# Optimization experiments

Measured on AMD Instinct MI355X. Metric: run time of the kernel, lower is better.

Reference implementation:

```python
import jax, jax.numpy as jnp
import numpy as np

B, Q, K, H, DQ, DK, DV = 16, 128, 512, 128, 128, 128, 128
MASK_VALUE = -1000000.0  # matches d2l.sequence_mask fill value


def setup_inputs() -> dict:
    key = jax.random.key(0)
    ks = jax.random.split(key, 7)
    queries = jax.random.normal(ks[0], (B, Q, DQ), dtype=jnp.float32)
    keys = jax.random.normal(ks[1], (B, K, DK), dtype=jnp.float32)
    values = jax.random.normal(ks[2], (B, K, DV), dtype=jnp.float32)
    valid_lens = jax.random.randint(ks[3], (B,), 1, K + 1, dtype=jnp.int32)
    # Linear params (no bias), scaled like torch default init ~ 1/sqrt(fan_in)
    W_q = jax.random.normal(ks[4], (DQ, H), dtype=jnp.float32) / np.sqrt(DQ)
    W_k = jax.random.normal(ks[5], (DK, H), dtype=jnp.float32) / np.sqrt(DK)
    w_v = jax.random.normal(ks[6], (H,), dtype=jnp.float32) / np.sqrt(H)
    return {"queries": queries, "keys": keys, "values": values,
            "valid_lens": valid_lens, "W_q": W_q, "W_k": W_k, "w_v": w_v}


def reference(queries, keys, values, valid_lens, W_q, W_k, w_v):
    # Project queries and keys: (B,Q,H), (B,K,H)
    q = jnp.einsum("bqd,dh->bqh", queries, W_q)
    k = jnp.einsum("bkd,dh->bkh", keys, W_k)
    # Broadcast add -> tanh -> linear-to-1 score: (B,Q,K)
    features = jnp.tanh(q[:, :, None, :] + k[:, None, :, :])  # (B,Q,K,H)
    scores = jnp.einsum("bqkh,h->bqk", features, w_v)
    # masked softmax over last axis; valid_lens is (B,), broadcast over Q
    mask = jnp.arange(K)[None, None, :] < valid_lens[:, None, None]  # (B,1,K)
    scores = jnp.where(mask, scores, MASK_VALUE)
    attn = jax.nn.softmax(scores, axis=-1)
    # weighted sum over keys: (B,Q,DV)
    return jnp.einsum("bqk,bkv->bqv", attn, values)
```

## Files before the change

### kernel.cpp

```cpp
#include <hip/hip_runtime.h>

#define NB 16
#define NQ 128
#define NK 512
#define NH 128
#define NDV 128

#define KPAD 132

typedef __attribute__((ext_vector_type(8))) short short8;
typedef __attribute__((ext_vector_type(4))) float f32x4;
typedef __attribute__((ext_vector_type(2))) float f32x2;

#define C2LOG2E 2.8853900817779268f
#define LOG2E   1.4426950408889634f

__device__ __forceinline__ short f2bf(float x) {
    unsigned u = __float_as_uint(x);
    unsigned r = (u + 0x7fffu + ((u >> 16) & 1u)) >> 16;
    return (short)r;
}
__device__ __forceinline__ float bf2f(short s) {
    return __uint_as_float(((unsigned)(unsigned short)s) << 16);
}


__global__ __launch_bounds__(256) void wsplit_kernel(
    const float* __restrict__ Wq, const float* __restrict__ Wk,
    const float* __restrict__ wv,
    short* __restrict__ pqh, short* __restrict__ pql,
    short* __restrict__ pkh, short* __restrict__ pkl,
    float* __restrict__ w2)
{
    int blk = blockIdx.x;
    int t   = threadIdx.x;
    if (blk == 0 && t < NH) w2[t] = 2.0f * wv[t];
    int w = blk >> 3, ht = blk & 7;
    int ks = t >> 6, lane = t & 63;
    int m = lane & 15, quad = lane >> 4;
    const float* W = w ? Wk : Wq;
    short* ph = w ? pkh : pqh;
    short* pl = w ? pkl : pql;
    short8 hi, lo;
#pragma unroll
    for (int j = 0; j < 8; ++j) {
        float x = W[(size_t)(ks * 32 + quad * 8 + j) * NH + ht * 16 + m];
        short h = f2bf(x);
        hi[j] = h;
        lo[j] = f2bf(x - bf2f(h));
    }
    size_t o = (size_t)((ht * 4 + ks) * 64 + lane) * 8;
    *(short8*)(ph + o) = hi;
    *(short8*)(pl + o) = lo;
}

__global__ __launch_bounds__(256) void proj_kernel(
    const float* __restrict__ Xq, const float* __restrict__ Xk,
    const short* __restrict__ pqh, const short* __restrict__ pql,
    const short* __restrict__ pkh, const short* __restrict__ pkl,
    float* __restrict__ Eq, float* __restrict__ Ek)
{
    __shared__ float s_x[16 * KPAD];

    int blk = blockIdx.x;
    const float* X; const short* ph; const short* pl; float* Y; int row0;
    if (blk < 128) { X = Xq; ph = pqh; pl = pql; Y = Eq; row0 = blk * 16; }
    else           { X = Xk; ph = pkh; pl = pkl; Y = Ek; row0 = (blk - 128) * 16; }
    int t = threadIdx.x;
    int wave = t >> 6, lane = t & 63;
    int m = lane & 15, quad = lane >> 4;

#pragma unroll
    for (int r = 0; r < 2; ++r) {
        int i = (t + r * 256) * 4;
        int row = i >> 7, col = i & 127;
        *(f32x4*)&s_x[row * KPAD + col] =
            *(const f32x4*)&X[(size_t)(row0 + row) * NH + col];
    }
    __syncthreads();

    short8 AH[4], AL[4];
#pragma unroll
    for (int ks = 0; ks < 4; ++ks) {
        int base = m * KPAD + ks * 32 + quad * 8;
        f32x4 x0 = *(const f32x4*)&s_x[base];
        f32x4 x1 = *(const f32x4*)&s_x[base + 4];
#pragma unroll
        for (int j = 0; j < 4; ++j) {
            short h0 = f2bf(x0[j]);
            AH[ks][j] = h0; AL[ks][j] = f2bf(x0[j] - bf2f(h0));
            short h1 = f2bf(x1[j]);
            AH[ks][j + 4] = h1; AL[ks][j + 4] = f2bf(x1[j] - bf2f(h1));
        }
    }
#pragma unroll
    for (int hi = 0; hi < 2; ++hi) {
        int ht = wave * 2 + hi;
        f32x4 acc = {0.f, 0.f, 0.f, 0.f};
#pragma unroll
        for (int ks = 0; ks < 4; ++ks) {
            size_t o = (size_t)((ht * 4 + ks) * 64 + lane) * 8;
            short8 bh = *(const short8*)(ph + o);
            short8 bl = *(const short8*)(pl + o);
            acc = __builtin_amdgcn_mfma_f32_16x16x32_bf16(AH[ks], bl, acc, 0, 0, 0);
            acc = __builtin_amdgcn_mfma_f32_16x16x32_bf16(AL[ks], bh, acc, 0, 0, 0);
            acc = __builtin_amdgcn_mfma_f32_16x16x32_bf16(AH[ks], bh, acc, 0, 0, 0);
        }
#pragma unroll
        for (int r = 0; r < 4; ++r)
            Y[(size_t)(row0 + quad * 4 + r) * NH + ht * 16 + m] =
                __builtin_amdgcn_exp2f(acc[r] * C2LOG2E);
    }
}

__global__ __launch_bounds__(512) void score_kernel(
    const float* __restrict__ Eqp, const float* __restrict__ Ekp,
    const int* __restrict__ vlen, const float* __restrict__ w2,
    float* __restrict__ P)
{
    __shared__ float s_ek[128 * KPAD];
    __shared__ float s_eq[16 * NH];
    __shared__ float s_w2[NH];

    int blk = blockIdx.x;
    int b    = blk & 15;
    int rest = blk >> 4;
    int qt = rest & 7, kc = rest >> 3;
    int q0 = qt * 16, k0 = kc * 128;
    int t  = threadIdx.x;

    int nv = vlen[b];
    nv = max(1, min(NK, nv));
    float* Pb = P + ((size_t)b * NQ + q0) * NK;

    if (k0 >= nv) {
        int q = t >> 5, kk = (t & 31) * 4;
        f32x4 z = {0.f, 0.f, 0.f, 0.f};
        *(f32x4*)&Pb[(size_t)q * NK + k0 + kk] = z;
        return;
    }

    for (int i = t; i < 128 * 32; i += 512) {
        int row = i >> 5, c4 = i & 31;
        f32x4 v = *(const f32x4*)&Ekp[((size_t)b * NK + k0 + row) * NH + c4 * 4];
        if (k0 + row >= nv) {
            f32x4 z = {0.f, 0.f, 0.f, 0.f};
            v = z;
        }
        *(f32x4*)&s_ek[row * KPAD + c4 * 4] = v;
    }
    *(f32x4*)&s_eq[t * 4] =
        *(const f32x4*)&Eqp[((size_t)b * NQ + q0) * NH + t * 4];
    if (t < 32) *(f32x4*)&s_w2[t * 4] = *(const f32x4*)&w2[t * 4];
    __syncthreads();

    int lane = t & 63, w = t >> 6;
    int g = w & 3, hf = w >> 2;

    float s2 = s_w2[lane] + s_w2[lane + 64];
#pragma unroll
    for (int off = 32; off; off >>= 1) s2 += __shfl_xor(s2, off);
    float wsum = 0.5f * s2;

    const float* ek = &s_ek[(hf * 64 + lane) * KPAD];
    const float* e0 = &s_eq[(g * 4 + 0) * NH];
    const float* e1 = &s_eq[(g * 4 + 1) * NH];
    const float* e2 = &s_eq[(g * 4 + 2) * NH];
    const float* e3 = &s_eq[(g * 4 + 3) * NH];

    const f32x2 one2 = {1.0f, 1.0f};
    f32x2 v00 = {0.f, 0.f}, v01 = {0.f, 0.f};
    f32x2 v10 = {0.f, 0.f}, v11 = {0.f, 0.f};
    f32x2 v20 = {0.f, 0.f}, v21 = {0.f, 0.f};
    f32x2 v30 = {0.f, 0.f}, v31 = {0.f, 0.f};

#define PKSTEP(accv, qv, kv, wv)                                        \
    {                                                                   \
        f32x2 x = qv * kv + one2;                                       \
        float R = __builtin_amdgcn_rcpf(x[0] * x[1]);                   \
        f32x2 xs = {x[1], x[0]};                                        \
        accv += wv * (R * xs);                                          \
    }

#pragma unroll
    for (int hh = 0; hh < NH; hh += 8) {
        f32x4 kAv = *(const f32x4*)(ek + hh);
        f32x4 kBv = *(const f32x4*)(ek + hh + 4);
        f32x4 wAv = *(const f32x4*)(s_w2 + hh);
        f32x4 wBv = *(const f32x4*)(s_w2 + hh + 4);
        f32x2 kA0 = {kAv[0], kAv[1]}, kA1 = {kAv[2], kAv[3]};
        f32x2 kB0 = {kBv[0], kBv[1]}, kB1 = {kBv[2], kBv[3]};
        f32x2 wA0 = {wAv[0], wAv[1]}, wA1 = {wAv[2], wAv[3]};
        f32x2 wB0 = {wBv[0], wBv[1]}, wB1 = {wBv[2], wBv[3]};
        {
            f32x4 qa = *(const f32x4*)(e0 + hh), qb = *(const f32x4*)(e0 + hh + 4);
            f32x2 qa0 = {qa[0], qa[1]}, qa1 = {qa[2], qa[3]};
            f32x2 qb0 = {qb[0], qb[1]}, qb1 = {qb[2], qb[3]};
            PKSTEP(v00, qa0, kA0, wA0); PKSTEP(v01, qa1, kA1, wA1);
            PKSTEP(v00, qb0, kB0, wB0); PKSTEP(v01, qb1, kB1, wB1);
        }
        {
            f32x4 qa = *(const f32x4*)(e1 + hh), qb = *(const f32x4*)(e1 + hh + 4);
            f32x2 qa0 = {qa[0], qa[1]}, qa1 = {qa[2], qa[3]};
            f32x2 qb0 = {qb[0], qb[1]}, qb1 = {qb[2], qb[3]};
            PKSTEP(v10, qa0, kA0, wA0); PKSTEP(v11, qa1, kA1, wA1);
            PKSTEP(v10, qb0, kB0, wB0); PKSTEP(v11, qb1, kB1, wB1);
        }
        {
            f32x4 qa = *(const f32x4*)(e2 + hh), qb = *(const f32x4*)(e2 + hh + 4);
            f32x2 qa0 = {qa[0], qa[1]}, qa1 = {qa[2], qa[3]};
            f32x2 qb0 = {qb[0], qb[1]}, qb1 = {qb[2], qb[3]};
            PKSTEP(v20, qa0, kA0, wA0); PKSTEP(v21, qa1, kA1, wA1);
            PKSTEP(v20, qb0, kB0, wB0); PKSTEP(v21, qb1, kB1, wB1);
        }
        {
            f32x4 qa = *(const f32x4*)(e3 + hh), qb = *(const f32x4*)(e3 + hh + 4);
            f32x2 qa0 = {qa[0], qa[1]}, qa1 = {qa[2], qa[3]};
            f32x2 qb0 = {qb[0], qb[1]}, qb1 = {qb[2], qb[3]};
            PKSTEP(v30, qa0, kA0, wA0); PKSTEP(v31, qa1, kA1, wA1);
            PKSTEP(v30, qb0, kB0, wB0); PKSTEP(v31, qb1, kB1, wB1);
        }
    }
#undef PKSTEP
    float c0 = (v00[0] + v00[1]) + (v01[0] + v01[1]);
    float c1 = (v10[0] + v10[1]) + (v11[0] + v11[1]);
    float c2 = (v20[0] + v20[1]) + (v21[0] + v21[1]);
    float c3 = (v30[0] + v30[1]) + (v31[0] + v31[1]);
    int kg = k0 + hf * 64 + lane;
    bool valid = kg < nv;
    float p0 = valid ? __builtin_amdgcn_exp2f((wsum - c0) * LOG2E) : 0.f;
    float p1 = valid ? __builtin_amdgcn_exp2f((wsum - c1) * LOG2E) : 0.f;
    float p2 = valid ? __builtin_amdgcn_exp2f((wsum - c2) * LOG2E) : 0.f;
    float p3 = valid ? __builtin_amdgcn_exp2f((wsum - c3) * LOG2E) : 0.f;
    float* Pr = Pb + (size_t)(g * 4) * NK + kg;
    Pr[0 * NK] = p0;
    Pr[1 * NK] = p1;
    Pr[2 * NK] = p2;
    Pr[3 * NK] = p3;
}

__global__ __launch_bounds__(256) void av_kernel(
    const float* __restrict__ P, const float* __restrict__ V,
    const int* __restrict__ vlen, float* __restrict__ out)
{
    __shared__ float s_p[8 * NK];

    int blk = blockIdx.x;
    int b = blk & 15, qt = blk >> 4;
    int q0 = qt * 8;
    int t = threadIdx.x;

    int nv = vlen[b];
    nv = max(1, min(NK, nv));
    int kfl = nv & ~7;

    const f32x4* Pv = (const f32x4*)(P + ((size_t)b * NQ + q0) * NK);
#pragma unroll
    for (int r = 0; r < 4; ++r)
        ((f32x4*)s_p)[t + r * 256] = Pv[t + r * 256];
    __syncthreads();

    int lane = t & 63, w = t >> 6;
    int qa = w * 2, qb = qa + 1;
    const float* pa = &s_p[qa * NK];
    const float* pb = &s_p[qb * NK];

    f32x4 sa0 = *(const f32x4*)(pa + lane * 8);
    f32x4 sa1 = *(const f32x4*)(pa + lane * 8 + 4);
    f32x4 sb0 = *(const f32x4*)(pb + lane * 8);
    f32x4 sb1 = *(const f32x4*)(pb + lane * 8 + 4);
    float sa = ((sa0[0] + sa0[1]) + (sa0[2] + sa0[3])) +
               ((sa1[0] + sa1[1]) + (sa1[2] + sa1[3]));
    float sb = ((sb0[0] + sb0[1]) + (sb0[2] + sb0[3])) +
               ((sb1[0] + sb1[1]) + (sb1[2] + sb1[3]));
#pragma unroll
    for (int off = 32; off; off >>= 1) {
        sa += __shfl_xor(sa, off);
        sb += __shfl_xor(sb, off);
    }
    float ra = 1.0f / sa, rb = 1.0f / sb;

    int par = lane >> 5;
    int dl  = lane & 31;
    int dv0 = dl * 4;
    const float* Vb = V + (size_t)b * NK * NDV + dv0;
    f32x4 Oa = {0.f, 0.f, 0.f, 0.f};
    f32x4 Ob = {0.f, 0.f, 0.f, 0.f};
    for (int k = 0; k < kfl; k += 8) {
        f32x4 pA0 = *(const f32x4*)(pa + k);
        f32x4 pA1 = *(const f32x4*)(pa + k + 4);
        f32x4 pB0 = *(const f32x4*)(pb + k);
        f32x4 pB1 = *(const f32x4*)(pb + k + 4);
        f32x4 v0 = *(const f32x4*)(Vb + (size_t)(k + 0 + par) * NDV);
        f32x4 v1 = *(const f32x4*)(Vb + (size_t)(k + 2 + par) * NDV);
        f32x4 v2 = *(const f32x4*)(Vb + (size_t)(k + 4 + par) * NDV);
        f32x4 v3 = *(const f32x4*)(Vb + (size_t)(k + 6 + par) * NDV);
        float a0 = pA0[par], a1 = pA0[2 + par], a2 = pA1[par], a3 = pA1[2 + par];
        float b0 = pB0[par], b1 = pB0[2 + par], b2 = pB1[par], b3 = pB1[2 + par];
#pragma unroll
        for (int j = 0; j < 4; ++j) {
            Oa[j] = fmaf(a0, v0[j], Oa[j]); Ob[j] = fmaf(b0, v0[j], Ob[j]);
            Oa[j] = fmaf(a1, v1[j], Oa[j]); Ob[j] = fmaf(b1, v1[j], Ob[j]);
            Oa[j] = fmaf(a2, v2[j], Oa[j]); Ob[j] = fmaf(b2, v2[j], Ob[j]);
            Oa[j] = fmaf(a3, v3[j], Oa[j]); Ob[j] = fmaf(b3, v3[j], Ob[j]);
        }
    }
    if (nv & 7) {
        int k = kfl;
        f32x4 z4 = {0.f, 0.f, 0.f, 0.f};
        f32x4 pA0 = *(const f32x4*)(pa + k);
        f32x4 pA1 = *(const f32x4*)(pa + k + 4);
        f32x4 pB0 = *(const f32x4*)(pb + k);
        f32x4 pB1 = *(const f32x4*)(pb + k + 4);
        f32x4 v0 = *(const f32x4*)(Vb + (size_t)(k + 0 + par) * NDV);
        f32x4 v1 = *(const f32x4*)(Vb + (size_t)(k + 2 + par) * NDV);
        f32x4 v2 = *(const f32x4*)(Vb + (size_t)(k + 4 + par) * NDV);
        f32x4 v3 = *(const f32x4*)(Vb + (size_t)(k + 6 + par) * NDV);
        if (k + 0 + par >= nv) v0 = z4;
        if (k + 2 + par >= nv) v1 = z4;
        if (k + 4 + par >= nv) v2 = z4;
        if (k + 6 + par >= nv) v3 = z4;
        float a0 = pA0[par], a1 = pA0[2 + par], a2 = pA1[par], a3 = pA1[2 + par];
        float b0 = pB0[par], b1 = pB0[2 + par], b2 = pB1[par], b3 = pB1[2 + par];
#pragma unroll
        for (int j = 0; j < 4; ++j) {
            Oa[j] = fmaf(a0, v0[j], Oa[j]); Ob[j] = fmaf(b0, v0[j], Ob[j]);
            Oa[j] = fmaf(a1, v1[j], Oa[j]); Ob[j] = fmaf(b1, v1[j], Ob[j]);
            Oa[j] = fmaf(a2, v2[j], Oa[j]); Ob[j] = fmaf(b2, v2[j], Ob[j]);
            Oa[j] = fmaf(a3, v3[j], Oa[j]); Ob[j] = fmaf(b3, v3[j], Ob[j]);
        }
    }
#pragma unroll
    for (int j = 0; j < 4; ++j) {
        Oa[j] += __shfl_xor(Oa[j], 32);
        Ob[j] += __shfl_xor(Ob[j], 32);
    }
    if (par == 0) {
        f32x4 o = {Oa[0] * ra, Oa[1] * ra, Oa[2] * ra, Oa[3] * ra};
        *(f32x4*)&out[((size_t)b * NQ + q0 + qa) * NDV + dv0] = o;
    } else {
        f32x4 o = {Ob[0] * rb, Ob[1] * rb, Ob[2] * rb, Ob[3] * rb};
        *(f32x4*)&out[((size_t)b * NQ + q0 + qb) * NDV + dv0] = o;
    }
}

extern "C" void kernel_launch(void* const* d_in, const int* in_sizes, int n_in,
                              void* d_out, int out_size, void* d_ws, size_t ws_size,
                              hipStream_t stream) {
    const float* q  = (const float*)d_in[0];
    const float* ks = (const float*)d_in[1];
    const float* vs = (const float*)d_in[2];
    const int*   vl = (const int*)d_in[3];
    const float* wq = (const float*)d_in[4];
    const float* wk = (const float*)d_in[5];
    const float* wv = (const float*)d_in[6];

    float* Eq = (float*)d_ws;
    float* Ek = Eq + 2048 * 128;
    float* P  = Ek + (size_t)8192 * 128;
    float* w2 = P + (size_t)NB * NQ * NK;
    short* pqh = (short*)(w2 + 128);
    short* pql = pqh + 16384;
    short* pkh = pql + 16384;
    short* pkl = pkh + 16384;

    wsplit_kernel<<<16, 256, 0, stream>>>(wq, wk, wv, pqh, pql, pkh, pkl, w2);
    proj_kernel<<<640, 256, 0, stream>>>(q, ks, pqh, pql, pkh, pkl, Eq, Ek);
    score_kernel<<<512, 512, 0, stream>>>(Eq, Ek, vl, w2, P);
    av_kernel<<<256, 256, 0, stream>>>(P, vs, vl, (float*)d_out);
}
```

Baseline: 103.0 us.

## Split AV kernel's key loop across warps with shared-memory reduction

Restructures the attention-times-values kernel so each block handles 4 query rows with 8 warps. Each warp takes a strided slice of the key dimension and accumulates all 4 rows, and the partial results are reduced through shared memory before normalising by the row sums. This raises the block count and shortens each warp's serial key loop, aiming for better latency hiding and parallelism in the final stage. The cost is an extra shared-memory reduction, an extra barrier, and more registers per thread.

```diff
diff --git a/kernel.cpp b/kernel.cpp
--- a/kernel.cpp
+++ b/kernel.cpp
@@ -239,79 +239,92 @@
     Pr[3 * NK] = p3;
 }
 
-__global__ __launch_bounds__(256) void av_kernel(
+__global__ __launch_bounds__(512, 4) void av_kernel(
     const float* __restrict__ P, const float* __restrict__ V,
     const int* __restrict__ vlen, float* __restrict__ out)
 {
-    __shared__ float s_p[8 * NK];
+    __shared__ float s_p[4 * NK];
+    __shared__ float s_red[8 * 4 * 128];
+    __shared__ float s_rsum[4];
 
     int blk = blockIdx.x;
-    int b = blk & 15, qt = blk >> 4;
-    int q0 = qt * 8;
+    int b = blk & 15, qq = blk >> 4;
+    int q0 = qq * 4;
     int t = threadIdx.x;
 
     int nv = vlen[b];
     nv = max(1, min(NK, nv));
-    int kfl = nv & ~7;
 
     const f32x4* Pv = (const f32x4*)(P + ((size_t)b * NQ + q0) * NK);
-#pragma unroll
-    for (int r = 0; r < 4; ++r)
-        ((f32x4*)s_p)[t + r * 256] = Pv[t + r * 256];
+    ((f32x4*)s_p)[t] = Pv[t];
     __syncthreads();
 
     int lane = t & 63, w = t >> 6;
-    int qa = w * 2, qb = qa + 1;
-    const float* pa = &s_p[qa * NK];
-    const float* pb = &s_p[qb * NK];
-
-    f32x4 sa0 = *(const f32x4*)(pa + lane * 8);
-    f32x4 sa1 = *(const f32x4*)(pa + lane * 8 + 4);
-    f32x4 sb0 = *(const f32x4*)(pb + lane * 8);
-    f32x4 sb1 = *(const f32x4*)(pb + lane * 8 + 4);
-    float sa = ((sa0[0] + sa0[1]) + (sa0[2] + sa0[3])) +
-               ((sa1[0] + sa1[1]) + (sa1[2] + sa1[3]));
-    float sb = ((sb0[0] + sb0[1]) + (sb0[2] + sb0[3])) +
-               ((sb1[0] + sb1[1]) + (sb1[2] + sb1[3]));
-#pragma unroll
-    for (int off = 32; off; off >>= 1) {
-        sa += __shfl_xor(sa, off);
-        sb += __shfl_xor(sb, off);
-    }
-    float ra = 1.0f / sa, rb = 1.0f / sb;
+
+    if (w < 4) {
+        const float* pr = &s_p[w * NK];
+        f32x4 s0 = *(const f32x4*)(pr + lane * 8);
+        f32x4 s1 = *(const f32x4*)(pr + lane * 8 + 4);
+        float s = ((s0[0] + s0[1]) + (s0[2] + s0[3])) +
+                  ((s1[0] + s1[1]) + (s1[2] + s1[3]));
+#pragma unroll
+        for (int off = 32; off; off >>= 1) s += __shfl_xor(s, off);
+        if (lane == 0) s_rsum[w] = s;
+    }
 
     int par = lane >> 5;
     int dl  = lane & 31;
     int dv0 = dl * 4;
     const float* Vb = V + (size_t)b * NK * NDV + dv0;
+    const float* pa = &s_p[0 * NK];
+    const float* pb = &s_p[1 * NK];
+    const float* pc = &s_p[2 * NK];
+    const float* pd = &s_p[3 * NK];
     f32x4 Oa = {0.f, 0.f, 0.f, 0.f};
     f32x4 Ob = {0.f, 0.f, 0.f, 0.f};
-    for (int k = 0; k < kfl; k += 8) {
+    f32x4 Oc = {0.f, 0.f, 0.f, 0.f};
+    f32x4 Od = {0.f, 0.f, 0.f, 0.f};
+
+    int k = w * 8;
+    for (; k + 8 <= nv; k += 64) {
         f32x4 pA0 = *(const f32x4*)(pa + k);
         f32x4 pA1 = *(const f32x4*)(pa + k + 4);
         f32x4 pB0 = *(const f32x4*)(pb + k);
         f32x4 pB1 = *(const f32x4*)(pb + k + 4);
+        f32x4 pC0 = *(const f32x4*)(pc + k);
+        f32x4 pC1 = *(const f32x4*)(pc + k + 4);
+        f32x4 pD0 = *(const f32x4*)(pd + k);
+        f32x4 pD1 = *(const f32x4*)(pd + k + 4);
         f32x4 v0 = *(const f32x4*)(Vb + (size_t)(k + 0 + par) * NDV);
         f32x4 v1 = *(const f32x4*)(Vb + (size_t)(k + 2 + par) * NDV);
         f32x4 v2 = *(const f32x4*)(Vb + (size_t)(k + 4 + par) * NDV);
         f32x4 v3 = *(const f32x4*)(Vb + (size_t)(k + 6 + par) * NDV);
         float a0 = pA0[par], a1 = pA0[2 + par], a2 = pA1[par], a3 = pA1[2 + par];
         float b0 = pB0[par], b1 = pB0[2 + par], b2 = pB1[par], b3 = pB1[2 + par];
+        float c0 = pC0[par], c1 = pC0[2 + par], c2 = pC1[par], c3 = pC1[2 + par];
+        float d0 = pD0[par], d1 = pD0[2 + par], d2 = pD1[par], d3 = pD1[2 + par];
 #pragma unroll
         for (int j = 0; j < 4; ++j) {
             Oa[j] = fmaf(a0, v0[j], Oa[j]); Ob[j] = fmaf(b0, v0[j], Ob[j]);
+            Oc[j] = fmaf(c0, v0[j], Oc[j]); Od[j] = fmaf(d0, v0[j], Od[j]);
             Oa[j] = fmaf(a1, v1[j], Oa[j]); Ob[j] = fmaf(b1, v1[j], Ob[j]);
+            Oc[j] = fmaf(c1, v1[j], Oc[j]); Od[j] = fmaf(d1, v1[j], Od[j]);
             Oa[j] = fmaf(a2, v2[j], Oa[j]); Ob[j] = fmaf(b2, v2[j], Ob[j]);
+            Oc[j] = fmaf(c2, v2[j], Oc[j]); Od[j] = fmaf(d2, v2[j], Od[j]);
             Oa[j] = fmaf(a3, v3[j], Oa[j]); Ob[j] = fmaf(b3, v3[j], Ob[j]);
-        }
-    }
-    if (nv & 7) {
-        int k = kfl;
+            Oc[j] = fmaf(c3, v3[j], Oc[j]); Od[j] = fmaf(d3, v3[j], Od[j]);
+        }
+    }
+    if (k < nv) {
         f32x4 z4 = {0.f, 0.f, 0.f, 0.f};
         f32x4 pA0 = *(const f32x4*)(pa + k);
         f32x4 pA1 = *(const f32x4*)(pa + k + 4);
         f32x4 pB0 = *(const f32x4*)(pb + k);
         f32x4 pB1 = *(const f32x4*)(pb + k + 4);
+        f32x4 pC0 = *(const f32x4*)(pc + k);
+        f32x4 pC1 = *(const f32x4*)(pc + k + 4);
+        f32x4 pD0 = *(const f32x4*)(pd + k);
+        f32x4 pD1 = *(const f32x4*)(pd + k + 4);
         f32x4 v0 = *(const f32x4*)(Vb + (size_t)(k + 0 + par) * NDV);
         f32x4 v1 = *(const f32x4*)(Vb + (size_t)(k + 2 + par) * NDV);
         f32x4 v2 = *(const f32x4*)(Vb + (size_t)(k + 4 + par) * NDV);
@@ -322,26 +335,42 @@
         if (k + 6 + par >= nv) v3 = z4;
         float a0 = pA0[par], a1 = pA0[2 + par], a2 = pA1[par], a3 = pA1[2 + par];
         float b0 = pB0[par], b1 = pB0[2 + par], b2 = pB1[par], b3 = pB1[2 + par];
+        float c0 = pC0[par], c1 = pC0[2 + par], c2 = pC1[par], c3 = pC1[2 + par];
+        float d0 = pD0[par], d1 = pD0[2 + par], d2 = pD1[par], d3 = pD1[2 + par];
 #pragma unroll
         for (int j = 0; j < 4; ++j) {
             Oa[j] = fmaf(a0, v0[j], Oa[j]); Ob[j] = fmaf(b0, v0[j], Ob[j]);
+            Oc[j] = fmaf(c0, v0[j], Oc[j]); Od[j] = fmaf(d0, v0[j], Od[j]);
             Oa[j] = fmaf(a1, v1[j], Oa[j]); Ob[j] = fmaf(b1, v1[j], Ob[j]);
+            Oc[j] = fmaf(c1, v1[j], Oc[j]); Od[j] = fmaf(d1, v1[j], Od[j]);
             Oa[j] = fmaf(a2, v2[j], Oa[j]); Ob[j] = fmaf(b2, v2[j], Ob[j]);
+            Oc[j] = fmaf(c2, v2[j], Oc[j]); Od[j] = fmaf(d2, v2[j], Od[j]);
             Oa[j] = fmaf(a3, v3[j], Oa[j]); Ob[j] = fmaf(b3, v3[j], Ob[j]);
+            Oc[j] = fmaf(c3, v3[j], Oc[j]); Od[j] = fmaf(d3, v3[j], Od[j]);
         }
     }
 #pragma unroll
     for (int j = 0; j < 4; ++j) {
         Oa[j] += __shfl_xor(Oa[j], 32);
         Ob[j] += __shfl_xor(Ob[j], 32);
-    }
+        Oc[j] += __shfl_xor(Oc[j], 32);
+        Od[j] += __shfl_xor(Od[j], 32);
+    }
+    float* rb = &s_red[w * 512];
     if (par == 0) {
-        f32x4 o = {Oa[0] * ra, Oa[1] * ra, Oa[2] * ra, Oa[3] * ra};
-        *(f32x4*)&out[((size_t)b * NQ + q0 + qa) * NDV + dv0] = o;
+        *(f32x4*)&rb[0 * 128 + dv0] = Oa;
+        *(f32x4*)&rb[1 * 128 + dv0] = Ob;
     } else {
-        f32x4 o = {Ob[0] * rb, Ob[1] * rb, Ob[2] * rb, Ob[3] * rb};
-        *(f32x4*)&out[((size_t)b * NQ + q0 + qb) * NDV + dv0] = o;
-    }
+        *(f32x4*)&rb[2 * 128 + dv0] = Oc;
+        *(f32x4*)&rb[3 * 128 + dv0] = Od;
+    }
+    __syncthreads();
+
+    int row = t >> 7, dv = t & 127;
+    float s = 0.f;
+#pragma unroll
+    for (int ww = 0; ww < 8; ++ww) s += s_red[ww * 512 + row * 128 + dv];
+    out[((size_t)b * NQ + q0 + row) * NDV + dv] = s * (1.0f / s_rsum[row]);
 }
 
 extern "C" void kernel_launch(void* const* d_in, const int* in_sizes, int n_in,
@@ -367,5 +396,5 @@
     wsplit_kernel<<<16, 256, 0, stream>>>(wq, wk, wv, pqh, pql, pkh, pkl, w2);
     proj_kernel<<<640, 256, 0, stream>>>(q, ks, pqh, pql, pkh, pkl, Eq, Ek);
     score_kernel<<<512, 512, 0, stream>>>(Eq, Ek, vl, w2, P);
-    av_kernel<<<256, 256, 0, stream>>>(P, vs, vl, (float*)d_out);
-}
+    av_kernel<<<512, 512, 0, stream>>>(P, vs, vl, (float*)d_out);
+}
```

New measurement: 100.2 us. 1.03x faster.

## Fuse score and attention-value kernels to eliminate the intermediate probability matrix

Applied to the files above, without the earlier changes.

Merges the score and AV kernels into one kernel that loops over key chunks per block of 8 queries. Each chunk computes unnormalized probabilities into shared memory and accumulates them against V, with the denominator and output reduced across waves at the end. This removes the global P round trip and one launch. In exchange, each block reloads Ek for half as many queries, the score and AV phases are serialized within a block, and register pressure rises from the 8-query accumulators.

```diff
diff --git a/kernel.cpp b/kernel.cpp
--- a/kernel.cpp
+++ b/kernel.cpp
@@ -113,49 +113,33 @@
     }
 }
 
-__global__ __launch_bounds__(512) void score_kernel(
+__global__ __launch_bounds__(512, 4) void sav_kernel(
     const float* __restrict__ Eqp, const float* __restrict__ Ekp,
-    const int* __restrict__ vlen, const float* __restrict__ w2,
-    float* __restrict__ P)
+    const float* __restrict__ V, const int* __restrict__ vlen,
+    const float* __restrict__ w2, float* __restrict__ out)
 {
     __shared__ float s_ek[128 * KPAD];
-    __shared__ float s_eq[16 * NH];
+    __shared__ float s_eq[8 * NH];
     __shared__ float s_w2[NH];
+    __shared__ float s_p[8 * 128];
+    __shared__ float s_dp[16];
 
     int blk = blockIdx.x;
-    int b    = blk & 15;
-    int rest = blk >> 4;
-    int qt = rest & 7, kc = rest >> 3;
-    int q0 = qt * 16, k0 = kc * 128;
-    int t  = threadIdx.x;
+    int b = blk & 15, qt = blk >> 4;
+    int q0 = qt * 8;
+    int t = threadIdx.x;
+    int lane = t & 63, w = t >> 6;
+    int g = w & 3, hf = w >> 2;
 
     int nv = vlen[b];
     nv = max(1, min(NK, nv));
-    float* Pb = P + ((size_t)b * NQ + q0) * NK;
-
-    if (k0 >= nv) {
-        int q = t >> 5, kk = (t & 31) * 4;
-        f32x4 z = {0.f, 0.f, 0.f, 0.f};
-        *(f32x4*)&Pb[(size_t)q * NK + k0 + kk] = z;
-        return;
-    }
-
-    for (int i = t; i < 128 * 32; i += 512) {
-        int row = i >> 5, c4 = i & 31;
-        f32x4 v = *(const f32x4*)&Ekp[((size_t)b * NK + k0 + row) * NH + c4 * 4];
-        if (k0 + row >= nv) {
-            f32x4 z = {0.f, 0.f, 0.f, 0.f};
-            v = z;
-        }
-        *(f32x4*)&s_ek[row * KPAD + c4 * 4] = v;
-    }
-    *(f32x4*)&s_eq[t * 4] =
-        *(const f32x4*)&Eqp[((size_t)b * NQ + q0) * NH + t * 4];
-    if (t < 32) *(f32x4*)&s_w2[t * 4] = *(const f32x4*)&w2[t * 4];
+
+    if (t < 256)
+        *(f32x4*)&s_eq[t * 4] =
+            *(const f32x4*)&Eqp[((size_t)b * NQ + q0) * NH + t * 4];
+    else if (t < 288)
+        *(f32x4*)&s_w2[(t - 256) * 4] = *(const f32x4*)&w2[(t - 256) * 4];
     __syncthreads();
-
-    int lane = t & 63, w = t >> 6;
-    int g = w & 3, hf = w >> 2;
 
     float s2 = s_w2[lane] + s_w2[lane + 64];
 #pragma unroll
@@ -163,16 +147,33 @@
     float wsum = 0.5f * s2;
 
     const float* ek = &s_ek[(hf * 64 + lane) * KPAD];
-    const float* e0 = &s_eq[(g * 4 + 0) * NH];
-    const float* e1 = &s_eq[(g * 4 + 1) * NH];
-    const float* e2 = &s_eq[(g * 4 + 2) * NH];
-    const float* e3 = &s_eq[(g * 4 + 3) * NH];
-
+    const float* e0 = &s_eq[(2 * g + 0) * NH];
+    const float* e1 = &s_eq[(2 * g + 1) * NH];
+
+    int par = lane >> 5, dl = lane & 31;
+    int dv0 = dl * 4;
+    const float* Vb = V + (size_t)b * NK * NDV + dv0;
+
+    f32x4 O[8];
+#pragma unroll
+    for (int q = 0; q < 8; ++q) { f32x4 z = {0.f,0.f,0.f,0.f}; O[q] = z; }
+    float den0 = 0.f, den1 = 0.f;
     const f32x2 one2 = {1.0f, 1.0f};
-    f32x2 v00 = {0.f, 0.f}, v01 = {0.f, 0.f};
-    f32x2 v10 = {0.f, 0.f}, v11 = {0.f, 0.f};
-    f32x2 v20 = {0.f, 0.f}, v21 = {0.f, 0.f};
-    f32x2 v30 = {0.f, 0.f}, v31 = {0.f, 0.f};
+
+    for (int kc = 0; kc < 4; ++kc) {
+        int k0 = kc * 128;
+        if (k0 >= nv) break;
+
+        for (int i = t; i < 128 * 32; i += 512) {
+            int row = i >> 5, c4 = i & 31;
+            f32x4 v = *(const f32x4*)&Ekp[((size_t)b * NK + k0 + row) * NH + c4 * 4];
+            if (k0 + row >= nv) { f32x4 z = {0.f,0.f,0.f,0.f}; v = z; }
+            *(f32x4*)&s_ek[row * KPAD + c4 * 4] = v;
+        }
+        __syncthreads();
+
+        f32x2 v00 = {0.f,0.f}, v01 = {0.f,0.f};
+        f32x2 v10 = {0.f,0.f}, v11 = {0.f,0.f};
 
 #define PKSTEP(accv, qv, kv, wv)                                        \
     {                                                                   \
@@ -183,164 +184,99 @@
     }
 
 #pragma unroll
-    for (int hh = 0; hh < NH; hh += 8) {
-        f32x4 kAv = *(const f32x4*)(ek + hh);
-        f32x4 kBv = *(const f32x4*)(ek + hh + 4);
-        f32x4 wAv = *(const f32x4*)(s_w2 + hh);
-        f32x4 wBv = *(const f32x4*)(s_w2 + hh + 4);
-        f32x2 kA0 = {kAv[0], kAv[1]}, kA1 = {kAv[2], kAv[3]};
-        f32x2 kB0 = {kBv[0], kBv[1]}, kB1 = {kBv[2], kBv[3]};
-        f32x2 wA0 = {wAv[0], wAv[1]}, wA1 = {wAv[2], wAv[3]};
-        f32x2 wB0 = {wBv[0], wBv[1]}, wB1 = {wBv[2], wBv[3]};
-        {
-            f32x4 qa = *(const f32x4*)(e0 + hh), qb = *(const f32x4*)(e0 + hh + 4);
-            f32x2 qa0 = {qa[0], qa[1]}, qa1 = {qa[2], qa[3]};
-            f32x2 qb0 = {qb[0], qb[1]}, qb1 = {qb[2], qb[3]};
-            PKSTEP(v00, qa0, kA0, wA0); PKSTEP(v01, qa1, kA1, wA1);
-            PKSTEP(v00, qb0, kB0, wB0); PKSTEP(v01, qb1, kB1, wB1);
-        }
-        {
-            f32x4 qa = *(const f32x4*)(e1 + hh), qb = *(const f32x4*)(e1 + hh + 4);
-            f32x2 qa0 = {qa[0], qa[1]}, qa1 = {qa[2], qa[3]};
-            f32x2 qb0 = {qb[0], qb[1]}, qb1 = {qb[2], qb[3]};
-            PKSTEP(v10, qa0, kA0, wA0); PKSTEP(v11, qa1, kA1, wA1);
-            PKSTEP(v10, qb0, kB0, wB0); PKSTEP(v11, qb1, kB1, wB1);
-        }
-        {
-            f32x4 qa = *(const f32x4*)(e2 + hh), qb = *(const f32x4*)(e2 + hh + 4);
-            f32x2 qa0 = {qa[0], qa[1]}, qa1 = {qa[2], qa[3]};
-            f32x2 qb0 = {qb[0], qb[1]}, qb1 = {qb[2], qb[3]};
-            PKSTEP(v20, qa0, kA0, wA0); PKSTEP(v21, qa1, kA1, wA1);
-            PKSTEP(v20, qb0, kB0, wB0); PKSTEP(v21, qb1, kB1, wB1);
-        }
-        {
-            f32x4 qa = *(const f32x4*)(e3 + hh), qb = *(const f32x4*)(e3 + hh + 4);
-            f32x2 qa0 = {qa[0], qa[1]}, qa1 = {qa[2], qa[3]};
-            f32x2 qb0 = {qb[0], qb[1]}, qb1 = {qb[2], qb[3]};
-            PKSTEP(v30, qa0, kA0, wA0); PKSTEP(v31, qa1, kA1, wA1);
-            PKSTEP(v30, qb0, kB0, wB0); PKSTEP(v31, qb1, kB1, wB1);
-        }
-    }
+        for (int hh = 0; hh < NH; hh += 8) {
+            f32x4 kAv = *(const f32x4*)(ek + hh);
+            f32x4 kBv = *(const f32x4*)(ek + hh + 4);
+            f32x4 wAv = *(const f32x4*)(s_w2 + hh);
+            f32x4 wBv = *(const f32x4*)(s_w2 + hh + 4);
+            f32x2 kA0 = {kAv[0], kAv[1]}, kA1 = {kAv[2], kAv[3]};
+            f32x2 kB0 = {kBv[0], kBv[1]}, kB1 = {kBv[2], kBv[3]};
+            f32x2 wA0 = {wAv[0], wAv[1]}, wA1 = {wAv[2], wAv[3]};
+            f32x2 wB0 = {wBv[0], wBv[1]}, wB1 = {wBv[2], wBv[3]};
+            {
+                f32x4 qa = *(const f32x4*)(e0 + hh), qb = *(const f32x4*)(e0 + hh + 4);
+                f32x2 qa0 = {qa[0], qa[1]}, qa1 = {qa[2], qa[3]};
+                f32x2 qb0 = {qb[0], qb[1]}, qb1 = {qb[2], qb[3]};
+                PKSTEP(v00, qa0, kA0, wA0); PKSTEP(v01, qa1, kA1, wA1);
+                PKSTEP(v00, qb0, kB0, wB0); PKSTEP(v01, qb1, kB1, wB1);
+            }
+            {
+                f32x4 qa = *(const f32x4*)(e1 + hh), qb = *(const f32x4*)(e1 + hh + 4);
+                f32x2 qa0 = {qa[0], qa[1]}, qa1 = {qa[2], qa[3]};
+                f32x2 qb0 = {qb[0], qb[1]}, qb1 = {qb[2], qb[3]};
+                PKSTEP(v10, qa0, kA0, wA0); PKSTEP(v11, qa1, kA1, wA1);
+                PKSTEP(v10, qb0, kB0, wB0); PKSTEP(v11, qb1, kB1, wB1);
+            }
+        }
 #undef PKSTEP
-    float c0 = (v00[0] + v00[1]) + (v01[0] + v01[1]);
-    float c1 = (v10[0] + v10[1]) + (v11[0] + v11[1]);
-    float c2 = (v20[0] + v20[1]) + (v21[0] + v21[1]);
-    float c3 = (v30[0] + v30[1]) + (v31[0] + v31[1]);
-    int kg = k0 + hf * 64 + lane;
-    bool valid = kg < nv;
-    float p0 = valid ? __builtin_amdgcn_exp2f((wsum - c0) * LOG2E) : 0.f;
-    float p1 = valid ? __builtin_amdgcn_exp2f((wsum - c1) * LOG2E) : 0.f;
-    float p2 = valid ? __builtin_amdgcn_exp2f((wsum - c2) * LOG2E) : 0.f;
-    float p3 = valid ? __builtin_amdgcn_exp2f((wsum - c3) * LOG2E) : 0.f;
-    float* Pr = Pb + (size_t)(g * 4) * NK + kg;
-    Pr[0 * NK] = p0;
-    Pr[1 * NK] = p1;
-    Pr[2 * NK] = p2;
-    Pr[3 * NK] = p3;
-}
-
-__global__ __launch_bounds__(256) void av_kernel(
-    const float* __restrict__ P, const float* __restrict__ V,
-    const int* __restrict__ vlen, float* __restrict__ out)
-{
-    __shared__ float s_p[8 * NK];
-
-    int blk = blockIdx.x;
-    int b = blk & 15, qt = blk >> 4;
-    int q0 = qt * 8;
-    int t = threadIdx.x;
-
-    int nv = vlen[b];
-    nv = max(1, min(NK, nv));
-    int kfl = nv & ~7;
-
-    const f32x4* Pv = (const f32x4*)(P + ((size_t)b * NQ + q0) * NK);
-#pragma unroll
-    for (int r = 0; r < 4; ++r)
-        ((f32x4*)s_p)[t + r * 256] = Pv[t + r * 256];
+        float c0 = (v00[0] + v00[1]) + (v01[0] + v01[1]);
+        float c1 = (v10[0] + v10[1]) + (v11[0] + v11[1]);
+        int kg = k0 + hf * 64 + lane;
+        bool valid = kg < nv;
+        float p0 = valid ? __builtin_amdgcn_exp2f((wsum - c0) * LOG2E) : 0.f;
+        float p1 = valid ? __builtin_amdgcn_exp2f((wsum - c1) * LOG2E) : 0.f;
+        s_p[(2 * g + 0) * 128 + hf * 64 + lane] = p0;
+        s_p[(2 * g + 1) * 128 + hf * 64 + lane] = p1;
+        float d0 = p0, d1 = p1;
+#pragma unroll
+        for (int off = 32; off; off >>= 1) {
+            d0 += __shfl_xor(d0, off);
+            d1 += __shfl_xor(d1, off);
+        }
+        den0 += d0; den1 += d1;
+        __syncthreads();
+
+        for (int m = 0; m < 2; ++m) {
+            int kk = w * 8 + m * 64;
+            int kg2 = k0 + kk;
+            if (kg2 >= nv) break;
+            f32x4 v0 = *(const f32x4*)(Vb + (size_t)(kg2 + 0 + par) * NDV);
+            f32x4 v1 = *(const f32x4*)(Vb + (size_t)(kg2 + 2 + par) * NDV);
+            f32x4 v2 = *(const f32x4*)(Vb + (size_t)(kg2 + 4 + par) * NDV);
+            f32x4 v3 = *(const f32x4*)(Vb + (size_t)(kg2 + 6 + par) * NDV);
+            if (kg2 + 8 > nv) {
+                f32x4 z4 = {0.f,0.f,0.f,0.f};
+                if (kg2 + 0 + par >= nv) v0 = z4;
+                if (kg2 + 2 + par >= nv) v1 = z4;
+                if (kg2 + 4 + par >= nv) v2 = z4;
+                if (kg2 + 6 + par >= nv) v3 = z4;
+            }
+#pragma unroll
+            for (int q = 0; q < 8; ++q) {
+                f32x4 pq0 = *(const f32x4*)&s_p[q * 128 + kk];
+                f32x4 pq1 = *(const f32x4*)&s_p[q * 128 + kk + 4];
+                float a0 = pq0[par], a1 = pq0[2 + par];
+                float a2 = pq1[par], a3 = pq1[2 + par];
+#pragma unroll
+                for (int j = 0; j < 4; ++j) {
+                    O[q][j] = fmaf(a0, v0[j], O[q][j]);
+                    O[q][j] = fmaf(a1, v1[j], O[q][j]);
+                    O[q][j] = fmaf(a2, v2[j], O[q][j]);
+                    O[q][j] = fmaf(a3, v3[j], O[q][j]);
+                }
+            }
+        }
+        __syncthreads();
+    }
+
+    float* s_red = s_ek;
+    int slot = w * 2 + par;
+#pragma unroll
+    for (int q = 0; q < 8; ++q)
+        *(f32x4*)&s_red[slot * 1024 + q * 128 + dv0] = O[q];
+    if (lane == 0) {
+        s_dp[hf * 8 + 2 * g]     = den0;
+        s_dp[hf * 8 + 2 * g + 1] = den1;
+    }
     __syncthreads();
 
-    int lane = t & 63, w = t >> 6;
-    int qa = w * 2, qb = qa + 1;
-    const float* pa = &s_p[qa * NK];
-    const float* pb = &s_p[qb * NK];
-
-    f32x4 sa0 = *(const f32x4*)(pa + lane * 8);
-    f32x4 sa1 = *(const f32x4*)(pa + lane * 8 + 4);
-    f32x4 sb0 = *(const f32x4*)(pb + lane * 8);
-    f32x4 sb1 = *(const f32x4*)(pb + lane * 8 + 4);
-    float sa = ((sa0[0] + sa0[1]) + (sa0[2] + sa0[3])) +
-               ((sa1[0] + sa1[1]) + (sa1[2] + sa1[3]));
-    float sb = ((sb0[0] + sb0[1]) + (sb0[2] + sb0[3])) +
-               ((sb1[0] + sb1[1]) + (sb1[2] + sb1[3]));
-#pragma unroll
-    for (int off = 32; off; off >>= 1) {
-        sa += __shfl_xor(sa, off);
-        sb += __shfl_xor(sb, off);
-    }
-    float ra = 1.0f / sa, rb = 1.0f / sb;
-
-    int par = lane >> 5;
-    int dl  = lane & 31;
-    int dv0 = dl * 4;
-    const float* Vb = V + (size_t)b * NK * NDV + dv0;
-    f32x4 Oa = {0.f, 0.f, 0.f, 0.f};
-    f32x4 Ob = {0.f, 0.f, 0.f, 0.f};
-    for (int k = 0; k < kfl; k += 8) {
-        f32x4 pA0 = *(const f32x4*)(pa + k);
-        f32x4 pA1 = *(const f32x4*)(pa + k + 4);
-        f32x4 pB0 = *(const f32x4*)(pb + k);
-        f32x4 pB1 = *(const f32x4*)(pb + k + 4);
-        f32x4 v0 = *(const f32x4*)(Vb + (size_t)(k + 0 + par) * NDV);
-        f32x4 v1 = *(const f32x4*)(Vb + (size_t)(k + 2 + par) * NDV);
-        f32x4 v2 = *(const f32x4*)(Vb + (size_t)(k + 4 + par) * NDV);
-        f32x4 v3 = *(const f32x4*)(Vb + (size_t)(k + 6 + par) * NDV);
-        float a0 = pA0[par], a1 = pA0[2 + par], a2 = pA1[par], a3 = pA1[2 + par];
-        float b0 = pB0[par], b1 = pB0[2 + par], b2 = pB1[par], b3 = pB1[2 + par];
-#pragma unroll
-        for (int j = 0; j < 4; ++j) {
-            Oa[j] = fmaf(a0, v0[j], Oa[j]); Ob[j] = fmaf(b0, v0[j], Ob[j]);
-            Oa[j] = fmaf(a1, v1[j], Oa[j]); Ob[j] = fmaf(b1, v1[j], Ob[j]);
-            Oa[j] = fmaf(a2, v2[j], Oa[j]); Ob[j] = fmaf(b2, v2[j], Ob[j]);
-            Oa[j] = fmaf(a3, v3[j], Oa[j]); Ob[j] = fmaf(b3, v3[j], Ob[j]);
-        }
-    }
-    if (nv & 7) {
-        int k = kfl;
-        f32x4 z4 = {0.f, 0.f, 0.f, 0.f};
-        f32x4 pA0 = *(const f32x4*)(pa + k);
-        f32x4 pA1 = *(const f32x4*)(pa + k + 4);
-        f32x4 pB0 = *(const f32x4*)(pb + k);
-        f32x4 pB1 = *(const f32x4*)(pb + k + 4);
-        f32x4 v0 = *(const f32x4*)(Vb + (size_t)(k + 0 + par) * NDV);
-        f32x4 v1 = *(const f32x4*)(Vb + (size_t)(k + 2 + par) * NDV);
-        f32x4 v2 = *(const f32x4*)(Vb + (size_t)(k + 4 + par) * NDV);
-        f32x4 v3 = *(const f32x4*)(Vb + (size_t)(k + 6 + par) * NDV);
-        if (k + 0 + par >= nv) v0 = z4;
-        if (k + 2 + par >= nv) v1 = z4;
-        if (k + 4 + par >= nv) v2 = z4;
-        if (k + 6 + par >= nv) v3 = z4;
-        float a0 = pA0[par], a1 = pA0[2 + par], a2 = pA1[par], a3 = pA1[2 + par];
-        float b0 = pB0[par], b1 = pB0[2 + par], b2 = pB1[par], b3 = pB1[2 + par];
-#pragma unroll
-        for (int j = 0; j < 4; ++j) {
-            Oa[j] = fmaf(a0, v0[j], Oa[j]); Ob[j] = fmaf(b0, v0[j], Ob[j]);
-            Oa[j] = fmaf(a1, v1[j], Oa[j]); Ob[j] = fmaf(b1, v1[j], Ob[j]);
-            Oa[j] = fmaf(a2, v2[j], Oa[j]); Ob[j] = fmaf(b2, v2[j], Ob[j]);
-            Oa[j] = fmaf(a3, v3[j], Oa[j]); Ob[j] = fmaf(b3, v3[j], Ob[j]);
-        }
-    }
-#pragma unroll
-    for (int j = 0; j < 4; ++j) {
-        Oa[j] += __shfl_xor(Oa[j], 32);
-        Ob[j] += __shfl_xor(Ob[j], 32);
-    }
-    if (par == 0) {
-        f32x4 o = {Oa[0] * ra, Oa[1] * ra, Oa[2] * ra, Oa[3] * ra};
-        *(f32x4*)&out[((size_t)b * NQ + q0 + qa) * NDV + dv0] = o;
-    } else {
-        f32x4 o = {Ob[0] * rb, Ob[1] * rb, Ob[2] * rb, Ob[3] * rb};
-        *(f32x4*)&out[((size_t)b * NQ + q0 + qb) * NDV + dv0] = o;
+    for (int i = t; i < 1024; i += 512) {
+        int row = i >> 7, dv = i & 127;
+        float s = 0.f;
+#pragma unroll
+        for (int sl = 0; sl < 16; ++sl) s += s_red[sl * 1024 + row * 128 + dv];
+        float den = s_dp[row] + s_dp[8 + row];
+        out[((size_t)b * NQ + q0 + row) * NDV + dv] = s * (1.0f / den);
     }
 }
 
@@ -357,8 +293,7 @@
 
     float* Eq = (float*)d_ws;
     float* Ek = Eq + 2048 * 128;
-    float* P  = Ek + (size_t)8192 * 128;
-    float* w2 = P + (size_t)NB * NQ * NK;
+    float* w2 = Ek + (size_t)8192 * 128;
     short* pqh = (short*)(w2 + 128);
     short* pql = pqh + 16384;
     short* pkh = pql + 16384;
@@ -366,6 +301,5 @@
 
     wsplit_kernel<<<16, 256, 0, stream>>>(wq, wk, wv, pqh, pql, pkh, pkl, w2);
     proj_kernel<<<640, 256, 0, stream>>>(q, ks, pqh, pql, pkh, pkl, Eq, Ek);
-    score_kernel<<<512, 512, 0, stream>>>(Eq, Ek, vl, w2, P);
-    av_kernel<<<256, 256, 0, stream>>>(P, vs, vl, (float*)d_out);
-}
+    sav_kernel<<<256, 512, 0, stream>>>(Eq, Ek, vs, vl, w2, (float*)d_out);
+}
```

Result: slower. 109.0 us (+5.9%).
